# Kernel tuning notes

Measured on AMD Instinct MI355X. Metric: run time of the kernel, lower is better.

Reference implementation:

```python
import jax, jax.numpy as jnp
import numpy as np

B, D = 65536, 1024
E, U, T = 10, 10, 2  # experts, expert units, tasks


def setup_inputs() -> dict:
    key = jax.random.key(0)
    ks = jax.random.split(key, 8)
    s = 0.02
    return {
        "x": jax.random.normal(ks[0], (B, D), dtype=jnp.float32),
        "show_index": jax.random.randint(ks[1], (B,), 0, 100),
        "st": jax.random.normal(ks[2], (B, 16), dtype=jnp.float32),
        "expert_w": jax.random.normal(ks[3], (E, D, U), dtype=jnp.float32) * s,
        "expert_b": jnp.zeros((E, U), dtype=jnp.float32),
        "gate_w": jax.random.normal(ks[4], (T, D, E), dtype=jnp.float32) * s,
        "gate_b": jnp.zeros((T, E), dtype=jnp.float32),
        "ctr_w": jax.random.normal(ks[5], (U, 1), dtype=jnp.float32) * s,
        "ctr_b": jnp.zeros((1,), dtype=jnp.float32),
        "cvr_w": jax.random.normal(ks[6], (U, 1), dtype=jnp.float32) * s,
        "cvr_b": jnp.zeros((1,), dtype=jnp.float32),
    }


def reference(x, show_index, st, expert_w, expert_b, gate_w, gate_b,
              ctr_w, ctr_b, cvr_w, cvr_b):
    # experts_output[b, u, e] = relu(x @ W_e + b_e)  (stacked on axis 2)
    experts_output = jax.nn.relu(
        jnp.einsum("bd,edu->bue", x, expert_w) + expert_b.T[None, :, :]
    )  # [B, U, E]
    # gates[b, t, e] = softmax over experts
    gates = jax.nn.softmax(
        jnp.einsum("bd,tde->bte", x, gate_w) + gate_b[None, :, :], axis=-1
    )  # [B, T, E]
    # weighted sum over experts for each task: [B, T, U]
    task_inputs = jnp.einsum("bue,bte->btu", experts_output, gates)
    ctr_logits = jax.nn.sigmoid(task_inputs[:, 0, :] @ ctr_w + ctr_b)  # [B, 1]
    cvr_logits = jax.nn.sigmoid(task_inputs[:, 1, :] @ cvr_w + cvr_b)  # [B, 1]
    return (ctr_logits, cvr_logits)
```

## Files before the change

kernel.cpp:

```cpp
#include <hip/hip_runtime.h>
#include <hip/hip_bf16.h>

#define B_ROWS 65536
#define D_DIM  1024
#define NC     120
#define CSTR   121

typedef __attribute__((ext_vector_type(4))) float f32x4;
typedef __attribute__((ext_vector_type(8))) short bf16x8;

__device__ __forceinline__ unsigned short f2bf(float f) {
  union { float f; unsigned u; } v; v.f = f;
  unsigned r = v.u + 0x7FFFu + ((v.u >> 16) & 1u);
  return (unsigned short)(r >> 16);
}

__device__ __forceinline__ short f2bfs(float f) {
  __hip_bfloat16 h = __float2bfloat16(f);
  return (short)__builtin_bit_cast(unsigned short, h);
}

__global__ __launch_bounds__(256) void pack_w(const float* __restrict__ ew,
                                              const float* __restrict__ gw,
                                              short* __restrict__ wt) {
  int idx = blockIdx.x * 256 + threadIdx.x;
  int c = idx >> 10, d = idx & 1023;
  float v = 0.f;
  if (c < 100) {
    int e = c / 10, u = c % 10;
    v = ew[(e * D_DIM + d) * 10 + u];
  } else if (c < NC) {
    int q = c - 100; int t = q / 10, e = q % 10;
    v = gw[(t * D_DIM + d) * 10 + e];
  }
  wt[c * D_DIM + d] = (short)f2bf(v);
}

__global__ __launch_bounds__(256, 2) void mmoe_main(
    const float* __restrict__ x, const short* __restrict__ wt,
    const float* __restrict__ eb, const float* __restrict__ gb,
    const float* __restrict__ ctr_w, const float* __restrict__ ctr_b,
    const float* __restrict__ cvr_w, const float* __restrict__ cvr_b,
    float* __restrict__ out) {
  __shared__ float C[4][32 * CSTR];
  const int tid  = threadIdx.x;
  const int wave = tid >> 6, lane = tid & 63;
  const int lhi  = lane >> 4, llo = lane & 15;
  const int m0   = blockIdx.x * 128 + wave * 32;

  const float* xr0 = x + (size_t)(m0 + llo) * D_DIM + lhi * 8;
  const float* xr1 = xr0 + (size_t)16 * D_DIM;
  const short* bb  = wt + llo * D_DIM + lhi * 8;

  f32x4 acc[2][8];
  #pragma unroll
  for (int rt = 0; rt < 2; ++rt)
    #pragma unroll
    for (int ct = 0; ct < 8; ++ct) acc[rt][ct] = (f32x4){0.f, 0.f, 0.f, 0.f};

  float4 pa[2][2][2];
  uint4  pb[2][8];

  pa[0][0][0] = *(const float4*)(xr0);
  pa[0][0][1] = *(const float4*)(xr0 + 4);
  pa[0][1][0] = *(const float4*)(xr1);
  pa[0][1][1] = *(const float4*)(xr1 + 4);
  #pragma unroll
  for (int ct = 0; ct < 8; ++ct)
    pb[0][ct] = *(const uint4*)(bb + ct * 16 * D_DIM);

  #pragma unroll 2
  for (int ks = 0; ks < 32; ++ks) {
    const int cur = ks & 1, nxt = cur ^ 1;
    const int kn = ((ks + 1) & 31) * 32;
    pa[nxt][0][0] = *(const float4*)(xr0 + kn);
    pa[nxt][0][1] = *(const float4*)(xr0 + kn + 4);
    pa[nxt][1][0] = *(const float4*)(xr1 + kn);
    pa[nxt][1][1] = *(const float4*)(xr1 + kn + 4);
    #pragma unroll
    for (int ct = 0; ct < 8; ++ct)
      pb[nxt][ct] = *(const uint4*)(bb + ct * 16 * D_DIM + kn);

    bf16x8 af[2];
    #pragma unroll
    for (int rt = 0; rt < 2; ++rt) {
      const float4 a = pa[cur][rt][0], b = pa[cur][rt][1];
      af[rt][0] = f2bfs(a.x); af[rt][1] = f2bfs(a.y);
      af[rt][2] = f2bfs(a.z); af[rt][3] = f2bfs(a.w);
      af[rt][4] = f2bfs(b.x); af[rt][5] = f2bfs(b.y);
      af[rt][6] = f2bfs(b.z); af[rt][7] = f2bfs(b.w);
    }
    #pragma unroll
    for (int ct = 0; ct < 8; ++ct) {
      const bf16x8 bf = __builtin_bit_cast(bf16x8, pb[cur][ct]);
      acc[0][ct] = __builtin_amdgcn_mfma_f32_16x16x32_bf16(af[0], bf, acc[0][ct], 0, 0, 0);
      acc[1][ct] = __builtin_amdgcn_mfma_f32_16x16x32_bf16(af[1], bf, acc[1][ct], 0, 0, 0);
    }
  }

  #pragma unroll
  for (int rt = 0; rt < 2; ++rt) {
    #pragma unroll
    for (int ct = 0; ct < 8; ++ct) {
      const int col = ct * 16 + llo;
      if (col < NC) {
        #pragma unroll
        for (int r = 0; r < 4; ++r)
          C[wave][(rt * 16 + lhi * 4 + r) * CSTR + col] = acc[rt][ct][r];
      }
    }
  }
  __syncthreads();

  {
    const int task = lane >> 5, row = lane & 31;
    const float* crow = &C[wave][row * CSTR];
    const float* tw = task ? cvr_w : ctr_w;
    const float tb = task ? cvr_b[0] : ctr_b[0];
    float s[10];
    #pragma unroll
    for (int e = 0; e < 10; ++e) {
      float a = 0.f;
      #pragma unroll
      for (int u = 0; u < 10; ++u) {
        float v = fmaxf(crow[e * 10 + u] + eb[e * 10 + u], 0.f);
        a = fmaf(v, tw[u], a);
      }
      s[e] = a;
    }
    float gl[10], mx = -1e30f;
    #pragma unroll
    for (int e = 0; e < 10; ++e) {
      gl[e] = crow[100 + task * 10 + e] + gb[task * 10 + e];
      mx = fmaxf(mx, gl[e]);
    }
    float den = 0.f, num = 0.f;
    #pragma unroll
    for (int e = 0; e < 10; ++e) {
      float pz = __expf(gl[e] - mx);
      den += pz; num = fmaf(pz, s[e], num);
    }
    const float z = num / den + tb;
    out[task * B_ROWS + m0 + row] = 1.f / (1.f + __expf(-z));
  }
}

extern "C" void kernel_launch(void* const* d_in, const int* in_sizes, int n_in,
                              void* d_out, int out_size, void* d_ws, size_t ws_size,
                              hipStream_t stream) {
  const float* x     = (const float*)d_in[0];
  const float* ew    = (const float*)d_in[3];
  const float* eb    = (const float*)d_in[4];
  const float* gw    = (const float*)d_in[5];
  const float* gb    = (const float*)d_in[6];
  const float* ctr_w = (const float*)d_in[7];
  const float* ctr_b = (const float*)d_in[8];
  const float* cvr_w = (const float*)d_in[9];
  const float* cvr_b = (const float*)d_in[10];
  float* out = (float*)d_out;
  short* wt  = (short*)d_ws;

  pack_w<<<512, 256, 0, stream>>>(ew, gw, wt);
  mmoe_main<<<B_ROWS / 128, 256, 0, stream>>>(x, wt, eb, gb, ctr_w, ctr_b,
                                              cvr_w, cvr_b, out);
}
```

Before: 412.4 us.

## Deepen x prefetch to three stages, coalesce weight pack, reverse block order

The main loop now prefetches x two k-steps ahead through a three-slot register ring, while the weight fragments stay double-buffered. The loop is fully unrolled and drops the wrap-around dummy load on the final iteration. The pack kernel now reads the expert and gate weights contiguously and scatters the bf16 writes, and zero-fills the padding columns separately. Blocks are traversed in reverse order, possibly to reuse x rows left in cache by an earlier launch. The deeper prefetch and full unroll add register pressure, which under launch_bounds(256,2) could cause spills.

```diff
diff --git a/kernel.cpp b/kernel.cpp
--- a/kernel.cpp
+++ b/kernel.cpp
@@ -24,16 +24,17 @@
                                               const float* __restrict__ gw,
                                               short* __restrict__ wt) {
   int idx = blockIdx.x * 256 + threadIdx.x;
-  int c = idx >> 10, d = idx & 1023;
-  float v = 0.f;
-  if (c < 100) {
-    int e = c / 10, u = c % 10;
-    v = ew[(e * D_DIM + d) * 10 + u];
-  } else if (c < NC) {
-    int q = c - 100; int t = q / 10, e = q % 10;
-    v = gw[(t * D_DIM + d) * 10 + e];
+  if (idx < 102400) {
+    int e = idx / 10240, r = idx % 10240, d = r / 10, u = r % 10;
+    wt[(e * 10 + u) * D_DIM + d] = (short)f2bf(ew[idx]);
+  } else if (idx < 122880) {
+    int j = idx - 102400;
+    int t = j / 10240, r = j % 10240, d = r / 10, e2 = r % 10;
+    wt[(100 + t * 10 + e2) * D_DIM + d] = (short)f2bf(gw[j]);
+  } else {
+    int j = idx - 122880;
+    wt[(120 + (j >> 10)) * D_DIM + (j & 1023)] = 0;
   }
-  wt[c * D_DIM + d] = (short)f2bf(v);
 }
 
 __global__ __launch_bounds__(256, 2) void mmoe_main(
@@ -46,7 +47,8 @@
   const int tid  = threadIdx.x;
   const int wave = tid >> 6, lane = tid & 63;
   const int lhi  = lane >> 4, llo = lane & 15;
-  const int m0   = blockIdx.x * 128 + wave * 32;
+  const int blk  = (int)gridDim.x - 1 - (int)blockIdx.x;
+  const int m0   = blk * 128 + wave * 32;
 
   const float* xr0 = x + (size_t)(m0 + llo) * D_DIM + lhi * 8;
   const float* xr1 = xr0 + (size_t)16 * D_DIM;
@@ -58,33 +60,42 @@
     #pragma unroll
     for (int ct = 0; ct < 8; ++ct) acc[rt][ct] = (f32x4){0.f, 0.f, 0.f, 0.f};
 
-  float4 pa[2][2][2];
+  float4 pa[3][2][2];
   uint4  pb[2][8];
 
   pa[0][0][0] = *(const float4*)(xr0);
   pa[0][0][1] = *(const float4*)(xr0 + 4);
   pa[0][1][0] = *(const float4*)(xr1);
   pa[0][1][1] = *(const float4*)(xr1 + 4);
+  pa[1][0][0] = *(const float4*)(xr0 + 32);
+  pa[1][0][1] = *(const float4*)(xr0 + 36);
+  pa[1][1][0] = *(const float4*)(xr1 + 32);
+  pa[1][1][1] = *(const float4*)(xr1 + 36);
   #pragma unroll
   for (int ct = 0; ct < 8; ++ct)
     pb[0][ct] = *(const uint4*)(bb + ct * 16 * D_DIM);
 
-  #pragma unroll 2
+  #pragma unroll
   for (int ks = 0; ks < 32; ++ks) {
-    const int cur = ks & 1, nxt = cur ^ 1;
-    const int kn = ((ks + 1) & 31) * 32;
-    pa[nxt][0][0] = *(const float4*)(xr0 + kn);
-    pa[nxt][0][1] = *(const float4*)(xr0 + kn + 4);
-    pa[nxt][1][0] = *(const float4*)(xr1 + kn);
-    pa[nxt][1][1] = *(const float4*)(xr1 + kn + 4);
-    #pragma unroll
-    for (int ct = 0; ct < 8; ++ct)
-      pb[nxt][ct] = *(const uint4*)(bb + ct * 16 * D_DIM + kn);
-
+    const int cur3 = ks % 3;
+    const int curb = ks & 1;
+    if (ks + 2 < 32) {
+      const int slot = (ks + 2) % 3, kn = (ks + 2) * 32;
+      pa[slot][0][0] = *(const float4*)(xr0 + kn);
+      pa[slot][0][1] = *(const float4*)(xr0 + kn + 4);
+      pa[slot][1][0] = *(const float4*)(xr1 + kn);
+      pa[slot][1][1] = *(const float4*)(xr1 + kn + 4);
+    }
+    if (ks + 1 < 32) {
+      const int kn = (ks + 1) * 32;
+      #pragma unroll
+      for (int ct = 0; ct < 8; ++ct)
+        pb[curb ^ 1][ct] = *(const uint4*)(bb + ct * 16 * D_DIM + kn);
+    }
     bf16x8 af[2];
     #pragma unroll
     for (int rt = 0; rt < 2; ++rt) {
-      const float4 a = pa[cur][rt][0], b = pa[cur][rt][1];
+      const float4 a = pa[cur3][rt][0], b = pa[cur3][rt][1];
       af[rt][0] = f2bfs(a.x); af[rt][1] = f2bfs(a.y);
       af[rt][2] = f2bfs(a.z); af[rt][3] = f2bfs(a.w);
       af[rt][4] = f2bfs(b.x); af[rt][5] = f2bfs(b.y);
@@ -92,9 +103,9 @@
     }
     #pragma unroll
     for (int ct = 0; ct < 8; ++ct) {
-      const bf16x8 bf = __builtin_bit_cast(bf16x8, pb[cur][ct]);
-      acc[0][ct] = __builtin_amdgcn_mfma_f32_16x16x32_bf16(af[0], bf, acc[0][ct], 0, 0, 0);
-      acc[1][ct] = __builtin_amdgcn_mfma_f32_16x16x32_bf16(af[1], bf, acc[1][ct], 0, 0, 0);
+      const bf16x8 bfr = __builtin_bit_cast(bf16x8, pb[curb][ct]);
+      acc[0][ct] = __builtin_amdgcn_mfma_f32_16x16x32_bf16(af[0], bfr, acc[0][ct], 0, 0, 0);
+      acc[1][ct] = __builtin_amdgcn_mfma_f32_16x16x32_bf16(af[1], bfr, acc[1][ct], 0, 0, 0);
     }
   }
 
```

New measurement: 423.4 us. 2.7% more time.
